# Kernel tuning notes

Hardware: AMD Instinct MI355X
Metric: run time of the kernel (lower is better)

## Reference

```python
import jax, jax.numpy as jnp
import numpy as np

N = 100000   # nodes
E = 1600000  # edges
D_IN = 7
H1 = 64
H2 = 32
G = 64       # graphs in batch


def setup_inputs() -> dict:
    key = jax.random.key(0)
    ks = jax.random.split(key, 10)
    x = jax.random.normal(ks[0], (N, D_IN), jnp.float32)
    edge_index = jax.random.randint(ks[1], (2, E), 0, N, dtype=jnp.int64)
    batch = jnp.sort(jax.random.randint(ks[2], (N,), 0, G, dtype=jnp.int64))
    # Glorot-style init for GCN weights
    W1 = jax.random.normal(ks[3], (D_IN, H1), jnp.float32) * (1.0 / np.sqrt(D_IN))
    b1 = jnp.zeros((H1,), jnp.float32)
    W2 = jax.random.normal(ks[4], (H1, H2), jnp.float32) * (1.0 / np.sqrt(H1))
    b2 = jnp.zeros((H2,), jnp.float32)
    W3 = jax.random.normal(ks[5], (H1, H2), jnp.float32) * (1.0 / np.sqrt(H1))
    b3 = jnp.zeros((H2,), jnp.float32)
    eps = jax.random.normal(ks[6], (N, H2), jnp.float32)  # reparam noise
    return dict(x=x, edge_index=edge_index, batch=batch,
                W1=W1, b1=b1, W2=W2, b2=b2, W3=W3, b3=b3, eps=eps)


def _gcn_agg(xw, src, dst, dis):
    # Symmetric-normalized aggregation with self-loops (PyG GCNConv default):
    # out[i] = sum_{(j->i)} d_i^{-1/2} d_j^{-1/2} xw[j] + d_i^{-1} xw[i]
    norm = (dis[src] * dis[dst])[:, None]
    msg = xw[src] * norm                      # [E, H] gather
    out = jax.ops.segment_sum(msg, dst, num_segments=N)  # scatter-add
    return out + xw * (dis * dis)[:, None]    # self-loop term


def reference(x, edge_index, batch, W1, b1, W2, b2, W3, b3, eps):
    src, dst = edge_index[0], edge_index[1]
    # degree on A + I (targets), unit edge weights
    deg = jax.ops.segment_sum(jnp.ones((E,), x.dtype), dst, num_segments=N) + 1.0
    dis = jax.lax.rsqrt(deg)  # deg^{-1/2}

    hidden1 = jax.nn.relu(_gcn_agg(x @ W1, src, dst, dis) + b1)

    # global mean pool of raw x over graphs
    counts = jax.ops.segment_sum(jnp.ones((N,), x.dtype), batch, num_segments=G)
    x_pooled = jax.ops.segment_sum(x, batch, num_segments=G) / jnp.maximum(counts, 1.0)[:, None]

    mu = jax.nn.relu(_gcn_agg(hidden1 @ W2, src, dst, dis) + b2)
    logvar = jax.nn.relu(_gcn_agg(hidden1 @ W3, src, dst, dis) + b3)

    # reparameterize: std = exp(logvar) (no 0.5 factor, as in source)
    z = eps * jnp.exp(logvar) + mu
    return z, x_pooled, mu, logvar
```

## Files before the change

kernel.cpp:

```cpp
#include <hip/hip_runtime.h>
#include <hip/hip_bf16.h>
#include <hip/hip_fp16.h>

#define NN 100000
#define NE 1600000
#define D_IN 7
#define H1 64
#define H2 32
#define NG 64
#define TE 2048
#define NTILE 782
#define BSH 9
#define NBUK 196
#define CAP 10240

typedef _Float16 f16x8 __attribute__((ext_vector_type(8)));
typedef float f32x4 __attribute__((ext_vector_type(4)));

__global__ void k_init(int* __restrict__ bucket_cursor) {
    int t = threadIdx.x;
    if (t < 256) bucket_cursor[t] = t * CAP;
}

__global__ __launch_bounds__(256) void k_bin(const int* __restrict__ src,
                                             const int* __restrict__ dst,
                                             int* __restrict__ bucket_cursor,
                                             int* __restrict__ staging) {
    __shared__ int hist[NBUK];
    __shared__ int startx[NBUK];
    __shared__ int runb[NBUK];
    __shared__ int cur[NBUK];
    __shared__ int sc[256];
    __shared__ int2 pairs[TE];
    int t = threadIdx.x;
    int base = blockIdx.x * TE;
    int tile_cnt = min(TE, NE - base);
    for (int i = t; i < NBUK; i += 256) hist[i] = 0;
    __syncthreads();
    int myd[TE / 256], mys[TE / 256];
#pragma unroll
    for (int k = 0; k < TE / 256; k++) {
        int i = base + k * 256 + t;
        if (i < NE) {
            myd[k] = dst[i]; mys[k] = src[i];
            atomicAdd(&hist[myd[k] >> BSH], 1);
        } else myd[k] = -1;
    }
    __syncthreads();
    int hv = (t < NBUK) ? hist[t] : 0;
    sc[t] = hv;
    __syncthreads();
    for (int off = 1; off < 256; off <<= 1) {
        int add = (t >= off) ? sc[t - off] : 0;
        __syncthreads();
        sc[t] += add;
        __syncthreads();
    }
    if (t < NBUK) {
        int ex = sc[t] - hv;
        startx[t] = ex;
        cur[t] = ex;
        if (hv > 0) runb[t] = atomicAdd(&bucket_cursor[t], hv);
    }
    __syncthreads();
#pragma unroll
    for (int k = 0; k < TE / 256; k++) {
        if (myd[k] >= 0) {
            int b = myd[k] >> BSH;
            int slot = atomicAdd(&cur[b], 1);
            pairs[slot] = make_int2(myd[k], mys[k]);
        }
    }
    __syncthreads();
    for (int i = t; i < tile_cnt; i += 256) {
        int2 p = pairs[i];
        int b = p.x >> BSH;
        staging[runb[b] + (i - startx[b])] = ((p.x & 511) << 17) | p.y;
    }
}

__global__ __launch_bounds__(512) void k_build(const int* __restrict__ staging,
                                               const int* __restrict__ bucket_cursor,
                                               int2* __restrict__ rowinfo,
                                               float* __restrict__ dis,
                                               int* __restrict__ csr,
                                               const float* __restrict__ x,
                                               float* __restrict__ xd8) {
    __shared__ int cnt[512];
    __shared__ int offs[512];
    __shared__ int cur[512];
    int t = threadIdx.x;
    int nbase = blockIdx.x << BSH;
    int ebase = blockIdx.x * CAP;
    int eend = bucket_cursor[blockIdx.x];
    cnt[t] = 0;
    __syncthreads();
    for (int i = ebase + t; i < eend; i += 512)
        atomicAdd(&cnt[staging[i] >> 17], 1);
    __syncthreads();
    int v = cnt[t];
    offs[t] = v;
    __syncthreads();
    for (int off = 1; off < 512; off <<= 1) {
        int add = (t >= off) ? offs[t - off] : 0;
        __syncthreads();
        offs[t] += add;
        __syncthreads();
    }
    int excl = offs[t] - v;
    cur[t] = excl;
    int node = nbase + t;
    if (node < NN) {
        rowinfo[node] = make_int2(ebase + excl, v);
        float d = rsqrtf((float)v + 1.0f);
        dis[node] = d;
        const float* xr = x + (size_t)node * D_IN;
        float4 w0 = make_float4(d * xr[0], d * xr[1], d * xr[2], d * xr[3]);
        float4 w1 = make_float4(d * xr[4], d * xr[5], d * xr[6], 0.f);
        float4* xo = (float4*)(xd8 + (size_t)node * 8);
        xo[0] = w0; xo[1] = w1;
    }
    __syncthreads();
    for (int i = ebase + t; i < eend; i += 512) {
        int p = staging[i];
        int pos = ebase + atomicAdd(&cur[p >> 17], 1);
        csr[pos] = p & 0x1FFFF;
    }
}

__device__ int lower_bound_i(const int* a, int n, int v) {
    int lo = 0, hi = n;
    while (lo < hi) { int mid = (lo + hi) >> 1; if (a[mid] < v) lo = mid + 1; else hi = mid; }
    return lo;
}

__global__ void k_pool(const float* __restrict__ x, const int* __restrict__ batch,
                       float* __restrict__ outp) {
    __shared__ int bounds[2];
    __shared__ float red[256 * D_IN];
    int g = blockIdx.x, t = threadIdx.x;
    if (t == 0) {
        bounds[0] = lower_bound_i(batch, NN, g);
        bounds[1] = lower_bound_i(batch, NN, g + 1);
    }
    __syncthreads();
    int s = bounds[0], e = bounds[1];
    float acc[D_IN];
#pragma unroll
    for (int k = 0; k < D_IN; k++) acc[k] = 0.f;
    for (int n = s + t; n < e; n += 256) {
#pragma unroll
        for (int k = 0; k < D_IN; k++) acc[k] += x[n * D_IN + k];
    }
#pragma unroll
    for (int k = 0; k < D_IN; k++) red[t * D_IN + k] = acc[k];
    __syncthreads();
    if (t < D_IN) {
        float sum = 0.f;
        for (int i = 0; i < 256; i++) sum += red[i * D_IN + t];
        float cnt = (float)(e - s);
        outp[g * D_IN + t] = sum / fmaxf(cnt, 1.f);
    }
}

__global__ __launch_bounds__(256) void k_aggx(const int2* __restrict__ rowinfo,
                                              const float* __restrict__ dis,
                                              const int* __restrict__ csr,
                                              const float* __restrict__ xd8,
                                              const float* __restrict__ W1,
                                              const float* __restrict__ b1,
                                              __half* __restrict__ h1h) {
    __shared__ float sW[D_IN * H1];
    __shared__ float sb[H1];
    __shared__ float sAx[64 * 9];
    int t = threadIdx.x;
    for (int i = t; i < D_IN * H1; i += 256) sW[i] = W1[i];
    if (t < H1) sb[t] = b1[t];
    int ll = t & 3;
    int ln = t >> 2;
    int node = blockIdx.x * 64 + ln;
    int nodec = min(node, NN - 1);
    int2 ri = rowinfo[nodec];
    int start = ri.x, c = ri.y;
    int cpos = start + max(c - 1, 0);
    int cmax = c;
    cmax = max(cmax, __shfl_xor(cmax, 4, 64));
    cmax = max(cmax, __shfl_xor(cmax, 8, 64));
    cmax = max(cmax, __shfl_xor(cmax, 16, 64));
    cmax = max(cmax, __shfl_xor(cmax, 32, 64));
    const float2* xb = (const float2*)xd8;
    float2 acc[4];
#pragma unroll
    for (int k = 0; k < 4; k++) acc[k] = make_float2(0.f, 0.f);
    for (int j = 0; j < cmax; j += 8) {
#pragma unroll
        for (int k = 0; k < 8; k++) {
            bool v = (j + k) < c;
            int s = csr[min(start + j + k, cpos)];
            s = v ? s : nodec;
            float2 r = xb[(size_t)s * 4 + ll];
            acc[k & 3].x += v ? r.x : 0.f;
            acc[k & 3].y += v ? r.y : 0.f;
        }
    }
    float sx = acc[0].x + acc[1].x + acc[2].x + acc[3].x;
    float sy = acc[0].y + acc[1].y + acc[2].y + acc[3].y;
    float2 self = xb[(size_t)nodec * 4 + ll];
    float dn = dis[nodec];
    sAx[ln * 9 + 2 * ll]     = dn * (sx + self.x);
    sAx[ln * 9 + 2 * ll + 1] = dn * (sy + self.y);
    __syncthreads();
    if (node < NN) {
        const float* axp = &sAx[ln * 9];
        union { __half h[16]; float4 f[2]; } u;
#pragma unroll
        for (int j = 0; j < 16; j++) {
            int h = ll * 16 + j;
            float a = sb[h];
#pragma unroll
            for (int k = 0; k < D_IN; k++) a += axp[k] * sW[k * H1 + h];
            u.h[j] = __float2half(dn * fmaxf(a, 0.f));
        }
        float4* d4 = (float4*)(h1h + (size_t)node * H1 + ll * 16);
        d4[0] = u.f[0];
        d4[1] = u.f[1];
    }
}

__global__ __launch_bounds__(256) void k_mm2mf(const __half* __restrict__ h1h,
                                               const float* __restrict__ W2,
                                               const float* __restrict__ W3,
                                               __half* __restrict__ y23h) {
    __shared__ __align__(16) _Float16 sW[64 * 80];
    int t = threadIdx.x;
    for (int i = t; i < 64 * 64; i += 256) {
        int c = i >> 6, k = i & 63;
        float w = (c < 32) ? W2[k * H2 + c] : W3[k * H2 + (c - 32)];
        sW[c * 80 + k] = (_Float16)w;
    }
    __syncthreads();
    int lane = t & 63;
    int c15 = lane & 15, k8 = lane >> 4;
    int r0 = blockIdx.x * 64 + (t >> 6) * 16;
    int row = r0 + c15;
    int rowc = min(row, NN - 1);
    const f16x8* hp = (const f16x8*)h1h;
    f16x8 a0 = hp[(size_t)rowc * 8 + k8];
    f16x8 a1 = hp[(size_t)rowc * 8 + k8 + 4];
    const _Float16* wb = sW + (size_t)c15 * 80 + k8 * 8;
    f16x8 b00 = *(const f16x8*)(wb);
    f16x8 b01 = *(const f16x8*)(wb + 32);
    f16x8 b10 = *(const f16x8*)(wb + 16 * 80);
    f16x8 b11 = *(const f16x8*)(wb + 16 * 80 + 32);
    f16x8 b20 = *(const f16x8*)(wb + 32 * 80);
    f16x8 b21 = *(const f16x8*)(wb + 32 * 80 + 32);
    f16x8 b30 = *(const f16x8*)(wb + 48 * 80);
    f16x8 b31 = *(const f16x8*)(wb + 48 * 80 + 32);
    f32x4 ac0 = {0.f, 0.f, 0.f, 0.f};
    f32x4 ac1 = ac0, ac2 = ac0, ac3 = ac0;
    ac0 = __builtin_amdgcn_mfma_f32_16x16x32_f16(a0, b00, ac0, 0, 0, 0);
    ac0 = __builtin_amdgcn_mfma_f32_16x16x32_f16(a1, b01, ac0, 0, 0, 0);
    ac1 = __builtin_amdgcn_mfma_f32_16x16x32_f16(a0, b10, ac1, 0, 0, 0);
    ac1 = __builtin_amdgcn_mfma_f32_16x16x32_f16(a1, b11, ac1, 0, 0, 0);
    ac2 = __builtin_amdgcn_mfma_f32_16x16x32_f16(a0, b20, ac2, 0, 0, 0);
    ac2 = __builtin_amdgcn_mfma_f32_16x16x32_f16(a1, b21, ac2, 0, 0, 0);
    ac3 = __builtin_amdgcn_mfma_f32_16x16x32_f16(a0, b30, ac3, 0, 0, 0);
    ac3 = __builtin_amdgcn_mfma_f32_16x16x32_f16(a1, b31, ac3, 0, 0, 0);
    int srow = r0 + k8 * 4;
#pragma unroll
    for (int i = 0; i < 4; i++) {
        int r = srow + i;
        if (r < NN) {
            __half* yr = y23h + (size_t)r * 64 + c15;
            yr[0]  = __float2half(ac0[i]);
            yr[16] = __float2half(ac1[i]);
            yr[32] = __float2half(ac2[i]);
            yr[48] = __float2half(ac3[i]);
        }
    }
}

__device__ __forceinline__ float4 h4_to_f4(float2 r) {
    __half2 h0 = *reinterpret_cast<__half2*>(&r.x);
    __half2 h1 = *reinterpret_cast<__half2*>(&r.y);
    float2 f0 = __half22float2(h0);
    float2 f1 = __half22float2(h1);
    return make_float4(f0.x, f0.y, f1.x, f1.y);
}

__device__ __forceinline__ void pk_acc_m(__half2& p, __half2& q, float2 r, bool v) {
    unsigned ux = v ? *reinterpret_cast<unsigned*>(&r.x) : 0u;
    unsigned uy = v ? *reinterpret_cast<unsigned*>(&r.y) : 0u;
    p = __hadd2(p, *reinterpret_cast<__half2*>(&ux));
    q = __hadd2(q, *reinterpret_cast<__half2*>(&uy));
}

__global__ __launch_bounds__(256) void k_agg2(const int2* __restrict__ rowinfo,
                                              const float* __restrict__ dis,
                                              const int* __restrict__ csr,
                                              const __half* __restrict__ y23h,
                                              const float* __restrict__ b2,
                                              const float* __restrict__ b3,
                                              const float* __restrict__ eps,
                                              float* __restrict__ out_z,
                                              float* __restrict__ out_mu,
                                              float* __restrict__ out_lv) {
    int t = threadIdx.x;
    int wave = (blockIdx.x * 256 + t) >> 6;
    int lane = t & 63;
    int sub = lane >> 4, l15 = lane & 15;
    int node = wave * 4 + sub;
    int2 ri = rowinfo[node];
    int start = ri.x, c = ri.y;
    int cpos = start + max(c - 1, 0);
    int cmax = c;
    cmax = max(cmax, __shfl_xor(cmax, 16, 64));
    cmax = max(cmax, __shfl_xor(cmax, 32, 64));
    const float2* yb = (const float2*)y23h;
    __half2 z2 = __float2half2_rn(0.f);
    __half2 p[4] = {z2, z2, z2, z2};
    __half2 q[4] = {z2, z2, z2, z2};
    for (int j = 0; j < cmax; j += 8) {
#pragma unroll
        for (int k = 0; k < 8; k++) {
            bool v = (j + k) < c;
            int s = csr[min(start + j + k, cpos)];
            s = v ? s : node;
            float2 r = yb[(size_t)s * 16 + l15];
            pk_acc_m(p[k & 3], q[k & 3], r, v);
        }
    }
    __half2 sp = __hadd2(__hadd2(p[0], p[1]), __hadd2(p[2], p[3]));
    __half2 sq = __hadd2(__hadd2(q[0], q[1]), __hadd2(q[2], q[3]));
    float2 fp = __half22float2(sp), fq = __half22float2(sq);
    float4 sv = h4_to_f4(yb[(size_t)node * 16 + l15]);
    float dn = dis[node];
    float4 bias = (l15 < 8) ? ((const float4*)b2)[l15] : ((const float4*)b3)[l15 - 8];
    float4 val;
    val.x = fmaxf(dn * (fp.x + sv.x) + bias.x, 0.f);
    val.y = fmaxf(dn * (fp.y + sv.y) + bias.y, 0.f);
    val.z = fmaxf(dn * (fq.x + sv.z) + bias.z, 0.f);
    val.w = fmaxf(dn * (fq.y + sv.w) + bias.w, 0.f);
    float4 other;
    other.x = __shfl_xor(val.x, 8, 64);
    other.y = __shfl_xor(val.y, 8, 64);
    other.z = __shfl_xor(val.z, 8, 64);
    other.w = __shfl_xor(val.w, 8, 64);
    if (l15 < 8) {
        size_t qi = (size_t)node * 8 + l15;
        ((float4*)out_mu)[qi] = val;
        float4 ev = ((const float4*)eps)[qi];
        float4 zz;
        zz.x = ev.x * __expf(other.x) + val.x;
        zz.y = ev.y * __expf(other.y) + val.y;
        zz.z = ev.z * __expf(other.z) + val.z;
        zz.w = ev.w * __expf(other.w) + val.w;
        ((float4*)out_z)[qi] = zz;
    } else {
        ((float4*)out_lv)[(size_t)node * 8 + (l15 - 8)] = val;
    }
}

extern "C" void kernel_launch(void* const* d_in, const int* in_sizes, int n_in,
                              void* d_out, int out_size, void* d_ws, size_t ws_size,
                              hipStream_t stream) {
    const float* x   = (const float*)d_in[0];
    const int*   ei  = (const int*)d_in[1];
    const int*   bat = (const int*)d_in[2];
    const float* W1  = (const float*)d_in[3];
    const float* b1  = (const float*)d_in[4];
    const float* W2  = (const float*)d_in[5];
    const float* b2  = (const float*)d_in[6];
    const float* W3  = (const float*)d_in[7];
    const float* b3  = (const float*)d_in[8];
    const float* eps = (const float*)d_in[9];

    const int* src = ei;
    const int* dst = ei + NE;

    float* out = (float*)d_out;
    float* out_z    = out;
    float* out_pool = out + (size_t)NN * H2;
    float* out_mu   = out_pool + NG * D_IN;
    float* out_lv   = out_mu + (size_t)NN * H2;

    int*    bucket_cursor = (int*)d_ws;
    int2*   rowinfo       = (int2*)(bucket_cursor + 256);
    float*  dis           = (float*)(rowinfo + NN);
    int*    staging       = (int*)(dis + NN);
    int*    csr           = staging + (size_t)NBUK * CAP;
    __half* h1h           = (__half*)(csr + (size_t)NBUK * CAP);
    __half* y23h          = h1h + (size_t)NN * H1;
    float*  xd8           = (float*)y23h;

    k_init  <<<1, 256, 0, stream>>>(bucket_cursor);
    k_bin   <<<NTILE, 256, 0, stream>>>(src, dst, bucket_cursor, staging);
    k_build <<<NBUK, 512, 0, stream>>>(staging, bucket_cursor, rowinfo, dis, csr, x, xd8);

    k_pool  <<<NG, 256, 0, stream>>>(x, bat, out_pool);

    k_aggx  <<<(NN + 63) / 64, 256, 0, stream>>>(rowinfo, dis, csr, xd8, W1, b1, h1h);
    k_mm2mf <<<(NN + 63) / 64, 256, 0, stream>>>(h1h, W2, W3, y23h);
    k_agg2  <<<NN / 16, 256, 0, stream>>>(rowinfo, dis, csr, y23h,
                                          b2, b3, eps, out_z, out_mu, out_lv);
}
```

Measured before the change: 213.0 us.

## Fuse layer-2 matmul into aggregation by aggregating hidden1 before projecting

```diff
diff --git a/kernel.cpp b/kernel.cpp
--- a/kernel.cpp
+++ b/kernel.cpp
@@ -17,9 +17,43 @@
 typedef _Float16 f16x8 __attribute__((ext_vector_type(8)));
 typedef float f32x4 __attribute__((ext_vector_type(4)));
 
-__global__ void k_init(int* __restrict__ bucket_cursor) {
-    int t = threadIdx.x;
-    if (t < 256) bucket_cursor[t] = t * CAP;
+__device__ int lower_bound_i(const int* a, int n, int v) {
+    int lo = 0, hi = n;
+    while (lo < hi) { int mid = (lo + hi) >> 1; if (a[mid] < v) lo = mid + 1; else hi = mid; }
+    return lo;
+}
+
+__global__ void k_pi(const float* __restrict__ x, const int* __restrict__ batch,
+                     float* __restrict__ outp, int* __restrict__ bucket_cursor) {
+    int g = blockIdx.x, t = threadIdx.x;
+    if (g == NG) {
+        if (t < 256) bucket_cursor[t] = t * CAP;
+        return;
+    }
+    __shared__ int bounds[2];
+    __shared__ float red[256 * D_IN];
+    if (t == 0) {
+        bounds[0] = lower_bound_i(batch, NN, g);
+        bounds[1] = lower_bound_i(batch, NN, g + 1);
+    }
+    __syncthreads();
+    int s = bounds[0], e = bounds[1];
+    float acc[D_IN];
+#pragma unroll
+    for (int k = 0; k < D_IN; k++) acc[k] = 0.f;
+    for (int n = s + t; n < e; n += 256) {
+#pragma unroll
+        for (int k = 0; k < D_IN; k++) acc[k] += x[n * D_IN + k];
+    }
+#pragma unroll
+    for (int k = 0; k < D_IN; k++) red[t * D_IN + k] = acc[k];
+    __syncthreads();
+    if (t < D_IN) {
+        float sum = 0.f;
+        for (int i = 0; i < 256; i++) sum += red[i * D_IN + t];
+        float cnt = (float)(e - s);
+        outp[g * D_IN + t] = sum / fmaxf(cnt, 1.f);
+    }
 }
 
 __global__ __launch_bounds__(256) void k_bin(const int* __restrict__ src,
@@ -30,7 +64,7 @@
     __shared__ int startx[NBUK];
     __shared__ int runb[NBUK];
     __shared__ int cur[NBUK];
-    __shared__ int sc[256];
+    __shared__ int wsum[4];
     __shared__ int2 pairs[TE];
     int t = threadIdx.x;
     int base = blockIdx.x * TE;
@@ -48,16 +82,20 @@
     }
     __syncthreads();
     int hv = (t < NBUK) ? hist[t] : 0;
-    sc[t] = hv;
-    __syncthreads();
-    for (int off = 1; off < 256; off <<= 1) {
-        int add = (t >= off) ? sc[t - off] : 0;
-        __syncthreads();
-        sc[t] += add;
-        __syncthreads();
-    }
+    int lane = t & 63, wv = t >> 6;
+    int sv = hv;
+#pragma unroll
+    for (int off = 1; off < 64; off <<= 1) {
+        int n = __shfl_up(sv, off, 64);
+        if (lane >= off) sv += n;
+    }
+    if (lane == 63) wsum[wv] = sv;
+    __syncthreads();
+    int wbase = 0;
+#pragma unroll
+    for (int i = 0; i < 4; i++) wbase += (i < wv) ? wsum[i] : 0;
     if (t < NBUK) {
-        int ex = sc[t] - hv;
+        int ex = wbase + sv - hv;
         startx[t] = ex;
         cur[t] = ex;
         if (hv > 0) runb[t] = atomicAdd(&bucket_cursor[t], hv);
@@ -87,8 +125,8 @@
                                                const float* __restrict__ x,
                                                float* __restrict__ xd8) {
     __shared__ int cnt[512];
-    __shared__ int offs[512];
     __shared__ int cur[512];
+    __shared__ int wsum[8];
     int t = threadIdx.x;
     int nbase = blockIdx.x << BSH;
     int ebase = blockIdx.x * CAP;
@@ -99,15 +137,19 @@
         atomicAdd(&cnt[staging[i] >> 17], 1);
     __syncthreads();
     int v = cnt[t];
-    offs[t] = v;
-    __syncthreads();
-    for (int off = 1; off < 512; off <<= 1) {
-        int add = (t >= off) ? offs[t - off] : 0;
-        __syncthreads();
-        offs[t] += add;
-        __syncthreads();
-    }
-    int excl = offs[t] - v;
+    int lane = t & 63, wv = t >> 6;
+    int sv = v;
+#pragma unroll
+    for (int off = 1; off < 64; off <<= 1) {
+        int n = __shfl_up(sv, off, 64);
+        if (lane >= off) sv += n;
+    }
+    if (lane == 63) wsum[wv] = sv;
+    __syncthreads();
+    int wbase = 0;
+#pragma unroll
+    for (int i = 0; i < 8; i++) wbase += (i < wv) ? wsum[i] : 0;
+    int excl = wbase + sv - v;
     cur[t] = excl;
     int node = nbase + t;
     if (node < NN) {
@@ -125,41 +167,6 @@
         int p = staging[i];
         int pos = ebase + atomicAdd(&cur[p >> 17], 1);
         csr[pos] = p & 0x1FFFF;
-    }
-}
-
-__device__ int lower_bound_i(const int* a, int n, int v) {
-    int lo = 0, hi = n;
-    while (lo < hi) { int mid = (lo + hi) >> 1; if (a[mid] < v) lo = mid + 1; else hi = mid; }
-    return lo;
-}
-
-__global__ void k_pool(const float* __restrict__ x, const int* __restrict__ batch,
-                       float* __restrict__ outp) {
-    __shared__ int bounds[2];
-    __shared__ float red[256 * D_IN];
-    int g = blockIdx.x, t = threadIdx.x;
-    if (t == 0) {
-        bounds[0] = lower_bound_i(batch, NN, g);
-        bounds[1] = lower_bound_i(batch, NN, g + 1);
-    }
-    __syncthreads();
-    int s = bounds[0], e = bounds[1];
-    float acc[D_IN];
-#pragma unroll
-    for (int k = 0; k < D_IN; k++) acc[k] = 0.f;
-    for (int n = s + t; n < e; n += 256) {
-#pragma unroll
-        for (int k = 0; k < D_IN; k++) acc[k] += x[n * D_IN + k];
-    }
-#pragma unroll
-    for (int k = 0; k < D_IN; k++) red[t * D_IN + k] = acc[k];
-    __syncthreads();
-    if (t < D_IN) {
-        float sum = 0.f;
-        for (int i = 0; i < 256; i++) sum += red[i * D_IN + t];
-        float cnt = (float)(e - s);
-        outp[g * D_IN + t] = sum / fmaxf(cnt, 1.f);
     }
 }
 
@@ -227,26 +234,86 @@
     }
 }
 
-__global__ __launch_bounds__(256) void k_mm2mf(const __half* __restrict__ h1h,
+__device__ __forceinline__ float4 h4_to_f4(float2 r) {
+    __half2 h0 = *reinterpret_cast<__half2*>(&r.x);
+    __half2 h1 = *reinterpret_cast<__half2*>(&r.y);
+    float2 f0 = __half22float2(h0);
+    float2 f1 = __half22float2(h1);
+    return make_float4(f0.x, f0.y, f1.x, f1.y);
+}
+
+__device__ __forceinline__ void pk_acc_m(__half2& p, __half2& q, float2 r, bool v) {
+    unsigned ux = v ? *reinterpret_cast<unsigned*>(&r.x) : 0u;
+    unsigned uy = v ? *reinterpret_cast<unsigned*>(&r.y) : 0u;
+    p = __hadd2(p, *reinterpret_cast<__half2*>(&ux));
+    q = __hadd2(q, *reinterpret_cast<__half2*>(&uy));
+}
+
+__global__ __launch_bounds__(256) void k_agg2f(const int2* __restrict__ rowinfo,
+                                               const float* __restrict__ dis,
+                                               const int* __restrict__ csr,
+                                               const __half* __restrict__ h1h,
                                                const float* __restrict__ W2,
                                                const float* __restrict__ W3,
-                                               __half* __restrict__ y23h) {
+                                               const float* __restrict__ b2,
+                                               const float* __restrict__ b3,
+                                               const float* __restrict__ eps,
+                                               float* __restrict__ out_z,
+                                               float* __restrict__ out_mu,
+                                               float* __restrict__ out_lv) {
     __shared__ __align__(16) _Float16 sW[64 * 80];
+    __shared__ __align__(16) _Float16 sT[64 * 72];
     int t = threadIdx.x;
     for (int i = t; i < 64 * 64; i += 256) {
         int c = i >> 6, k = i & 63;
         float w = (c < 32) ? W2[k * H2 + c] : W3[k * H2 + (c - 32)];
         sW[c * 80 + k] = (_Float16)w;
     }
-    __syncthreads();
     int lane = t & 63;
-    int c15 = lane & 15, k8 = lane >> 4;
-    int r0 = blockIdx.x * 64 + (t >> 6) * 16;
-    int row = r0 + c15;
-    int rowc = min(row, NN - 1);
-    const f16x8* hp = (const f16x8*)h1h;
-    f16x8 a0 = hp[(size_t)rowc * 8 + k8];
-    f16x8 a1 = hp[(size_t)rowc * 8 + k8 + 4];
+    int wv = t >> 6;
+    int sub = lane >> 4, l15 = lane & 15;
+    const float2* yb = (const float2*)h1h;
+    for (int g = 0; g < 4; g++) {
+        int lrow = wv * 16 + g * 4 + sub;
+        int node = blockIdx.x * 64 + lrow;
+        int nodec = min(node, NN - 1);
+        int2 ri = rowinfo[nodec];
+        int start = ri.x, c = ri.y;
+        int cpos = start + max(c - 1, 0);
+        int cmax = c;
+        cmax = max(cmax, __shfl_xor(cmax, 16, 64));
+        cmax = max(cmax, __shfl_xor(cmax, 32, 64));
+        __half2 z2 = __float2half2_rn(0.f);
+        __half2 p[4] = {z2, z2, z2, z2};
+        __half2 q[4] = {z2, z2, z2, z2};
+        for (int j = 0; j < cmax; j += 8) {
+#pragma unroll
+            for (int k = 0; k < 8; k++) {
+                bool v = (j + k) < c;
+                int s = csr[min(start + j + k, cpos)];
+                s = v ? s : nodec;
+                float2 r = yb[(size_t)s * 16 + l15];
+                pk_acc_m(p[k & 3], q[k & 3], r, v);
+            }
+        }
+        __half2 sp = __hadd2(__hadd2(p[0], p[1]), __hadd2(p[2], p[3]));
+        __half2 sq = __hadd2(__hadd2(q[0], q[1]), __hadd2(q[2], q[3]));
+        float2 fp = __half22float2(sp), fq = __half22float2(sq);
+        float4 sv = h4_to_f4(yb[(size_t)nodec * 16 + l15]);
+        float dn = dis[nodec];
+        __half2 ha, hb;
+        ha.x = __float2half(dn * (fp.x + sv.x)); ha.y = __float2half(dn * (fp.y + sv.y));
+        hb.x = __float2half(dn * (fq.x + sv.z)); hb.y = __float2half(dn * (fq.y + sv.w));
+        float2 st;
+        st.x = *reinterpret_cast<float*>(&ha);
+        st.y = *reinterpret_cast<float*>(&hb);
+        *(float2*)&sT[lrow * 72 + l15 * 4] = st;
+    }
+    __syncthreads();
+    int c15 = l15, k8 = sub;
+    const _Float16* ap = &sT[(wv * 16 + c15) * 72];
+    f16x8 a0 = *(const f16x8*)(ap + k8 * 8);
+    f16x8 a1 = *(const f16x8*)(ap + 32 + k8 * 8);
     const _Float16* wb = sW + (size_t)c15 * 80 + k8 * 8;
     f16x8 b00 = *(const f16x8*)(wb);
     f16x8 b01 = *(const f16x8*)(wb + 32);
@@ -266,98 +333,26 @@
     ac2 = __builtin_amdgcn_mfma_f32_16x16x32_f16(a1, b21, ac2, 0, 0, 0);
     ac3 = __builtin_amdgcn_mfma_f32_16x16x32_f16(a0, b30, ac3, 0, 0, 0);
     ac3 = __builtin_amdgcn_mfma_f32_16x16x32_f16(a1, b31, ac3, 0, 0, 0);
-    int srow = r0 + k8 * 4;
+    float bb2a = b2[c15], bb2b = b2[c15 + 16];
+    float bb3a = b3[c15], bb3b = b3[c15 + 16];
+    int srow = blockIdx.x * 64 + wv * 16 + k8 * 4;
 #pragma unroll
     for (int i = 0; i < 4; i++) {
         int r = srow + i;
         if (r < NN) {
-            __half* yr = y23h + (size_t)r * 64 + c15;
-            yr[0]  = __float2half(ac0[i]);
-            yr[16] = __float2half(ac1[i]);
-            yr[32] = __float2half(ac2[i]);
-            yr[48] = __float2half(ac3[i]);
-        }
-    }
-}
-
-__device__ __forceinline__ float4 h4_to_f4(float2 r) {
-    __half2 h0 = *reinterpret_cast<__half2*>(&r.x);
-    __half2 h1 = *reinterpret_cast<__half2*>(&r.y);
-    float2 f0 = __half22float2(h0);
-    float2 f1 = __half22float2(h1);
-    return make_float4(f0.x, f0.y, f1.x, f1.y);
-}
-
-__device__ __forceinline__ void pk_acc_m(__half2& p, __half2& q, float2 r, bool v) {
-    unsigned ux = v ? *reinterpret_cast<unsigned*>(&r.x) : 0u;
-    unsigned uy = v ? *reinterpret_cast<unsigned*>(&r.y) : 0u;
-    p = __hadd2(p, *reinterpret_cast<__half2*>(&ux));
-    q = __hadd2(q, *reinterpret_cast<__half2*>(&uy));
-}
-
-__global__ __launch_bounds__(256) void k_agg2(const int2* __restrict__ rowinfo,
-                                              const float* __restrict__ dis,
-                                              const int* __restrict__ csr,
-                                              const __half* __restrict__ y23h,
-                                              const float* __restrict__ b2,
-                                              const float* __restrict__ b3,
-                                              const float* __restrict__ eps,
-                                              float* __restrict__ out_z,
-                                              float* __restrict__ out_mu,
-                                              float* __restrict__ out_lv) {
-    int t = threadIdx.x;
-    int wave = (blockIdx.x * 256 + t) >> 6;
-    int lane = t & 63;
-    int sub = lane >> 4, l15 = lane & 15;
-    int node = wave * 4 + sub;
-    int2 ri = rowinfo[node];
-    int start = ri.x, c = ri.y;
-    int cpos = start + max(c - 1, 0);
-    int cmax = c;
-    cmax = max(cmax, __shfl_xor(cmax, 16, 64));
-    cmax = max(cmax, __shfl_xor(cmax, 32, 64));
-    const float2* yb = (const float2*)y23h;
-    __half2 z2 = __float2half2_rn(0.f);
-    __half2 p[4] = {z2, z2, z2, z2};
-    __half2 q[4] = {z2, z2, z2, z2};
-    for (int j = 0; j < cmax; j += 8) {
-#pragma unroll
-        for (int k = 0; k < 8; k++) {
-            bool v = (j + k) < c;
-            int s = csr[min(start + j + k, cpos)];
-            s = v ? s : node;
-            float2 r = yb[(size_t)s * 16 + l15];
-            pk_acc_m(p[k & 3], q[k & 3], r, v);
-        }
-    }
-    __half2 sp = __hadd2(__hadd2(p[0], p[1]), __hadd2(p[2], p[3]));
-    __half2 sq = __hadd2(__hadd2(q[0], q[1]), __hadd2(q[2], q[3]));
-    float2 fp = __half22float2(sp), fq = __half22float2(sq);
-    float4 sv = h4_to_f4(yb[(size_t)node * 16 + l15]);
-    float dn = dis[node];
-    float4 bias = (l15 < 8) ? ((const float4*)b2)[l15] : ((const float4*)b3)[l15 - 8];
-    float4 val;
-    val.x = fmaxf(dn * (fp.x + sv.x) + bias.x, 0.f);
-    val.y = fmaxf(dn * (fp.y + sv.y) + bias.y, 0.f);
-    val.z = fmaxf(dn * (fq.x + sv.z) + bias.z, 0.f);
-    val.w = fmaxf(dn * (fq.y + sv.w) + bias.w, 0.f);
-    float4 other;
-    other.x = __shfl_xor(val.x, 8, 64);
-    other.y = __shfl_xor(val.y, 8, 64);
-    other.z = __shfl_xor(val.z, 8, 64);
-    other.w = __shfl_xor(val.w, 8, 64);
-    if (l15 < 8) {
-        size_t qi = (size_t)node * 8 + l15;
-        ((float4*)out_mu)[qi] = val;
-        float4 ev = ((const float4*)eps)[qi];
-        float4 zz;
-        zz.x = ev.x * __expf(other.x) + val.x;
-        zz.y = ev.y * __expf(other.y) + val.y;
-        zz.z = ev.z * __expf(other.z) + val.z;
-        zz.w = ev.w * __expf(other.w) + val.w;
-        ((float4*)out_z)[qi] = zz;
-    } else {
-        ((float4*)out_lv)[(size_t)node * 8 + (l15 - 8)] = val;
+            float mu0 = fmaxf(ac0[i] + bb2a, 0.f);
+            float mu1 = fmaxf(ac1[i] + bb2b, 0.f);
+            float lv0 = fmaxf(ac2[i] + bb3a, 0.f);
+            float lv1 = fmaxf(ac3[i] + bb3b, 0.f);
+            size_t o0 = (size_t)r * 32 + c15;
+            float e0 = eps[o0], e1 = eps[o0 + 16];
+            out_mu[o0]      = mu0;
+            out_mu[o0 + 16] = mu1;
+            out_lv[o0]      = lv0;
+            out_lv[o0 + 16] = lv1;
+            out_z[o0]       = e0 * __expf(lv0) + mu0;
+            out_z[o0 + 16]  = e1 * __expf(lv1) + mu1;
+        }
     }
 }
 
@@ -390,17 +385,12 @@
     int*    staging       = (int*)(dis + NN);
     int*    csr           = staging + (size_t)NBUK * CAP;
     __half* h1h           = (__half*)(csr + (size_t)NBUK * CAP);
-    __half* y23h          = h1h + (size_t)NN * H1;
-    float*  xd8           = (float*)y23h;
-
-    k_init  <<<1, 256, 0, stream>>>(bucket_cursor);
+    float*  xd8           = (float*)(h1h + (size_t)NN * H1);
+
+    k_pi    <<<NG + 1, 256, 0, stream>>>(x, bat, out_pool, bucket_cursor);
     k_bin   <<<NTILE, 256, 0, stream>>>(src, dst, bucket_cursor, staging);
     k_build <<<NBUK, 512, 0, stream>>>(staging, bucket_cursor, rowinfo, dis, csr, x, xd8);
-
-    k_pool  <<<NG, 256, 0, stream>>>(x, bat, out_pool);
-
     k_aggx  <<<(NN + 63) / 64, 256, 0, stream>>>(rowinfo, dis, csr, xd8, W1, b1, h1h);
-    k_mm2mf <<<(NN + 63) / 64, 256, 0, stream>>>(h1h, W2, W3, y23h);
-    k_agg2  <<<NN / 16, 256, 0, stream>>>(rowinfo, dis, csr, y23h,
-                                          b2, b3, eps, out_z, out_mu, out_lv);
-}
+    k_agg2f <<<(NN + 63) / 64, 256, 0, stream>>>(rowinfo, dis, csr, h1h, W2, W3,
+                                                 b2, b3, eps, out_z, out_mu, out_lv);
+}
```

Result: no change. 210.7 us (-1.1%).
